# Kernel tuning notes

Hardware: AMD Instinct MI355X
Metric: run time of the kernel (lower is better)

Reference implementation:

```python
import jax, jax.numpy as jnp
import numpy as np

L = 3          # atom_decoder_depth
HEADS = 8      # spatial attention heads
T_HEADS = 8    # temporal attention heads
WQ = 32        # atoms_per_window_queries
HK = 128       # atoms_per_window_keys
EPS = 1e-5


def _ln(x, g=None, b=None):
    mu = jnp.mean(x, -1, keepdims=True)
    v = jnp.mean((x - mu) ** 2, -1, keepdims=True)
    xn = (x - mu) * jax.lax.rsqrt(v + EPS)
    if g is not None:
        xn = xn * g + b
    return xn


def _adaln(a, s, w_sc, b_sc, w_sk):
    # adaptive LN: sigmoid-scaled normed activations + conditioned skip
    sn = _ln(s)
    return jax.nn.sigmoid(sn @ w_sc + b_sc) * _ln(a) + sn @ w_sk


def setup_inputs() -> dict:
    key = jax.random.key(0)
    ks = iter(jax.random.split(key, 64))
    B0, T, N, M, D, TS = 1, 8, 1024, 4096, 256, 768
    HID = 2 * D

    def rn(shape, s=1.0):
        return jax.random.normal(next(ks), shape, jnp.float32) * s

    NW = (M + WQ - 1) // WQ
    a = rn((B0 * T, N, 2 * TS))
    q = rn((B0 * T, M, D))
    c = rn((B0 * T, M, D))
    atom_dec_bias = rn((B0, NW, WQ, HK, L * HEADS), 0.1)
    tok_idx = jnp.sort(jax.random.randint(next(ks), (B0, M), 0, N), axis=-1)
    atom_to_token = jax.nn.one_hot(tok_idx, N, dtype=jnp.float32)
    atom_pad_mask = jnp.ones((B0, M), bool)
    timestamps = jnp.sort(jax.random.uniform(next(ks), (B0, T)) * 10.0, axis=-1)
    p = 0.02
    return dict(
        a=a, q=q, c=c, atom_dec_bias=atom_dec_bias,
        atom_to_token=atom_to_token, atom_pad_mask=atom_pad_mask,
        timestamps=timestamps,
        W_a2q=rn((2 * TS, D), p),
        ada1_sw=rn((L, D, D), p), ada1_sb=rn((L, D), p), ada1_kw=rn((L, D, D), p),
        attn_wq=rn((L, D, D), p), attn_bq=rn((L, D), p),
        attn_wk=rn((L, D, D), p), attn_wv=rn((L, D, D), p),
        attn_wg=rn((L, D, D), p), attn_wo=rn((L, D, D), p),
        og_w=rn((L, D, D), p), og_b=rn((L, D), p),
        ada2_sw=rn((L, D, D), p), ada2_sb=rn((L, D), p), ada2_kw=rn((L, D, D), p),
        tr_w1=rn((L, D, HID), p), tr_w2=rn((L, D, HID), p), tr_w3=rn((L, HID, D), p),
        tr_gw=rn((L, D, D), p), tr_gb=rn((L, D), p),
        t_ln_g=jnp.ones((L, D)), t_ln_b=jnp.zeros((L, D)),
        t_wq=rn((L, D, D), p), t_wk=rn((L, D, D), p), t_wv=rn((L, D, D), p),
        t_wg=rn((L, D, D), p), t_wo=rn((L, D, D), p),
        t_decay=rn((L, T_HEADS)),
        pos_g=jnp.ones((D,)), pos_b=jnp.zeros((D,)), pos_w=rn((D, 3), p),
        T=8,
    )


def _forward(a, q, c, atom_dec_bias, atom_to_token, atom_pad_mask, timestamps,
             W_a2q, ada1_sw, ada1_sb, ada1_kw, attn_wq, attn_bq, attn_wk,
             attn_wv, attn_wg, attn_wo, og_w, og_b, ada2_sw, ada2_sb, ada2_kw,
             tr_w1, tr_w2, tr_w3, tr_gw, tr_gb, t_ln_g, t_ln_b, t_wq, t_wk,
             t_wv, t_wg, t_wo, t_decay, pos_g, pos_b, pos_w, T):
    BT, N, _ = a.shape
    B0 = BT // T
    M0, D = q.shape[1], q.shape[2]
    NW = (M0 + WQ - 1) // WQ
    M = NW * WQ
    h, dh = HEADS, D // HEADS
    th, tdh = T_HEADS, D // T_HEADS

    # token -> atom gather via one-hot matmul (atom_to_token shared across T)
    a2q = jnp.einsum('bmn,btnd->btmd', atom_to_token,
                     (a @ W_a2q).reshape(B0, T, N, D)).reshape(BT, M0, D)
    q = q + a2q

    pad = M - M0
    qf = jnp.pad(q, ((0, 0), (0, pad), (0, 0)))
    cf = jnp.pad(c, ((0, 0), (0, pad), (0, 0)))
    mask = jnp.pad(atom_pad_mask, ((0, 0), (0, pad)))  # (B0, M)

    side = (HK - WQ) // 2
    # index map: query window w attends keys [w*WQ - side, w*WQ - side + HK)
    widx = jnp.arange(NW)[:, None] * WQ + jnp.arange(HK)[None, :]

    def window_keys(x):  # (B, M, D) -> (B, NW, HK, D)
        xp = jnp.pad(x, ((0, 0), (side, side), (0, 0)))
        return xp[:, widx]

    kmask = jnp.pad(mask, ((0, 0), (side, side)))[:, widx]  # (B0, NW, HK)
    neg = jnp.where(kmask[:, None, :, None, None, :], 0.0, -1e9)

    bias = atom_dec_bias.reshape(B0, NW, WQ, HK, L, HEADS)
    inv_s = 1.0 / np.sqrt(dh).astype(np.float32)
    inv_t = 1.0 / np.sqrt(tdh).astype(np.float32)
    dt = jnp.abs(timestamps[:, :, None] - timestamps[:, None, :])  # (B0,T,T)

    for i in range(L):
        # ---- spatial windowed attention with pair bias ----
        b = _adaln(qf, cf, ada1_sw[i], ada1_sb[i], ada1_kw[i])
        qh = (b @ attn_wq[i] + attn_bq[i]).reshape(BT, NW, WQ, h, dh)
        kin = window_keys(b)                                   # (BT,NW,HK,D)
        kh = (kin @ attn_wk[i]).reshape(BT, NW, HK, h, dh)
        vh = (kin @ attn_wv[i]).reshape(BT, NW, HK, h, dh)
        logits = jnp.einsum('bnqhd,bnkhd->bnhqk', qh, kh) * inv_s
        logits = logits.reshape(B0, T, NW, h, WQ, HK)
        logits = logits + bias[:, :, :, :, i].transpose(0, 1, 4, 2, 3)[:, None] + neg
        p_attn = jax.nn.softmax(logits, axis=-1).reshape(BT, NW, h, WQ, HK)
        o = jnp.einsum('bnhqk,bnkhd->bnqhd', p_attn, vh)
        g = jax.nn.sigmoid(b @ attn_wg[i]).reshape(BT, NW, WQ, h, dh)
        o = (g * o).reshape(BT, M, D) @ attn_wo[i]
        qf = qf + jax.nn.sigmoid(cf @ og_w[i] + og_b[i]) * o
        # conditioned SwiGLU transition
        t = _adaln(qf, cf, ada2_sw[i], ada2_sb[i], ada2_kw[i])
        x = jax.nn.silu(t @ tr_w1[i]) * (t @ tr_w2[i])
        qf = qf + jax.nn.sigmoid(cf @ tr_gw[i] + tr_gb[i]) * (x @ tr_w3[i])
        # ---- temporal attention with per-head decay bias ----
        xt = qf.reshape(B0, T, M, D).transpose(0, 2, 1, 3)     # (B0,M,T,D)
        xn = _ln(xt, t_ln_g[i], t_ln_b[i])
        tq = (xn @ t_wq[i]).reshape(B0, M, T, th, tdh)
        tk = (xn @ t_wk[i]).reshape(B0, M, T, th, tdh)
        tv = (xn @ t_wv[i]).reshape(B0, M, T, th, tdh)
        tl = jnp.einsum('bmqhd,bmkhd->bmhqk', tq, tk) * inv_t
        decay = jax.nn.softplus(t_decay[i])                    # (th,)
        tl = tl - decay[None, None, :, None, None] * dt[:, None, None]
        tp = jax.nn.softmax(tl, axis=-1)
        to = jnp.einsum('bmhqk,bmkhd->bmqhd', tp, tv).reshape(B0, M, T, D)
        tg = jax.nn.sigmoid(xn @ t_wg[i])
        xt = xt + (tg * to) @ t_wo[i]
        qf = xt.transpose(0, 2, 1, 3).reshape(BT, M, D)

    q_out = qf[:, :M0]
    return _ln(q_out, pos_g, pos_b) @ pos_w  # (B*T, M0, 3)


def reference(a, q, c, atom_dec_bias, atom_to_token, atom_pad_mask, timestamps,
              W_a2q, ada1_sw, ada1_sb, ada1_kw, attn_wq, attn_bq, attn_wk,
              attn_wv, attn_wg, attn_wo, og_w, og_b, ada2_sw, ada2_sb, ada2_kw,
              tr_w1, tr_w2, tr_w3, tr_gw, tr_gb, t_ln_g, t_ln_b, t_wq, t_wk,
              t_wv, t_wg, t_wo, t_decay, pos_g, pos_b, pos_w, T):
    return _forward(a, q, c, atom_dec_bias, atom_to_token, atom_pad_mask,
                    timestamps, W_a2q, ada1_sw, ada1_sb, ada1_kw, attn_wq,
                    attn_bq, attn_wk, attn_wv, attn_wg, attn_wo, og_w, og_b,
                    ada2_sw, ada2_sb, ada2_kw, tr_w1, tr_w2, tr_w3, tr_gw,
                    tr_gb, t_ln_g, t_ln_b, t_wq, t_wk, t_wv, t_wg, t_wo,
                    t_decay, pos_g, pos_b, pos_w, T)
```

## Files before the change

### kernel.cpp

```cpp
#include <hip/hip_runtime.h>
#include <cstddef>
#include <cstdint>

#define DEVI __device__ __forceinline__

typedef __attribute__((ext_vector_type(8))) __bf16 bf16x8;
typedef __attribute__((ext_vector_type(8))) unsigned short us8;
typedef __attribute__((ext_vector_type(4))) unsigned short us4;
typedef __attribute__((ext_vector_type(4))) float f32x4;

constexpr int B0_ = 1, T_ = 8, N_ = 1024, M_ = 4096, D_ = 256;
constexpr int BT_ = 8, NW_ = 128, WQ_ = 32, HK_ = 128, SIDE_ = 48;
constexpr int R_ = BT_ * M_;
constexpr size_t Fq = 8388608;

DEVI unsigned short f2b(float f) {
  return __builtin_bit_cast(unsigned short, static_cast<__bf16>(f));
}
DEVI float b2f(unsigned short s) { return __uint_as_float(((unsigned)s) << 16); }
DEVI float sigm(float x) { return 1.0f / (1.0f + __expf(-x)); }
DEVI bf16x8 ld_bf8(const unsigned short* p) {
  return __builtin_bit_cast(bf16x8, *(const us8*)p);
}
DEVI bf16x8 pack_f8(float4 v0, float4 v1) {
  bf16x8 r;
  r[0] = (__bf16)v0.x; r[1] = (__bf16)v0.y; r[2] = (__bf16)v0.z; r[3] = (__bf16)v0.w;
  r[4] = (__bf16)v1.x; r[5] = (__bf16)v1.y; r[6] = (__bf16)v1.z; r[7] = (__bf16)v1.w;
  return r;
}
DEVI void mfma_bf16(f32x4& c, bf16x8 a, bf16x8 b) {
  c = __builtin_amdgcn_mfma_f32_16x16x32_bf16(a, b, c, 0, 0, 0);
}
DEVI void gload16(const void* g, void* l) {
  __builtin_amdgcn_global_load_lds((__attribute__((address_space(1))) void*)g,
                                   (__attribute__((address_space(3))) void*)l, 16, 0, 0);
}

struct ConvArgs {
  const float* src[64];
  int doff[64];
  int Kd[64];
  int Nd[64];
  int n;
};

__global__ __launch_bounds__(256) void conv_k(ConvArgs ca, unsigned short* __restrict__ wbf) {
  int e = blockIdx.x;
  int K = ca.Kd[e], N = ca.Nd[e];
  int nx = N >> 6, nk = K >> 6;
  int t = blockIdx.y;
  if (t >= nx * nk) return;
  int tx = t % nx, tk = t / nx;
  const float* s = ca.src[e];
  unsigned short* d = wbf + ca.doff[e];
  int n = tx * 64 + (threadIdx.x & 63);
  int k0 = tk * 64 + (threadIdx.x >> 6) * 16;
  for (int r = 0; r < 16; r++) {
    int k = k0 + r;
    d[(size_t)n * K + k] = f2b(s[(size_t)k * N + n]);
  }
}

__global__ __launch_bounds__(256) void cvt_k(const float* __restrict__ s,
                                             unsigned short* __restrict__ d, int n8) {
  int i = blockIdx.x * 256 + threadIdx.x;
  if (i >= n8) return;
  float4 v0 = *(const float4*)(s + (size_t)i * 8);
  float4 v1 = *(const float4*)(s + (size_t)i * 8 + 4);
  *(us8*)(d + (size_t)i * 8) = __builtin_bit_cast(us8, pack_f8(v0, v1));
}

__global__ __launch_bounds__(256) void bias_prep_k(
    const float* __restrict__ bq, const float* __restrict__ sb1,
    const float* __restrict__ sb2, const float* __restrict__ ogb,
    const float* __restrict__ trb, float* __restrict__ bias) {
  int t = threadIdx.x;
  for (int i = t; i < 1024 + 3 * 2560; i += 256) bias[i] = 0.f;
  __syncthreads();
  for (int i = 0; i < 3; i++) {
    float* B = bias + 1024 + i * 2560;
    B[t]        = bq[i * 256 + t];
    B[1024 + t] = sb1[i * 256 + t];
    B[1536 + t] = sb2[i * 256 + t];
    B[2048 + t] = ogb[i * 256 + t];
    B[2304 + t] = trb[i * 256 + t];
  }
}

__global__ __launch_bounds__(256) void biasb_k(const float* __restrict__ adb,
                                               unsigned short* __restrict__ biasb) {
  __shared__ float ld[3072];
  int rq = blockIdx.x;
  int t = threadIdx.x;
  const float* src = adb + (size_t)rq * 3072;
  for (int i = t; i < 3072; i += 256) ld[i] = src[i];
  __syncthreads();
  int k = t & 127;
  for (int lh = t >> 7; lh < 24; lh += 2)
    biasb[((size_t)lh * 4096 + rq) * 128 + k] = f2b(ld[k * 24 + lh]);
}

__global__ __launch_bounds__(256) void tokidx_k(const float* __restrict__ a2t,
                                                int* __restrict__ idx) {
  int m = blockIdx.x * 4 + (threadIdx.x >> 6);
  int lane = threadIdx.x & 63;
  int best = -1;
  for (int j = 0; j < 16; j++) {
    int col = lane * 16 + j;
    if (a2t[(size_t)m * 1024 + col] > 0.5f) best = col;
  }
#pragma unroll
  for (int off = 1; off < 64; off <<= 1) best = max(best, __shfl_xor(best, off));
  if (lane == 0) idx[m] = best;
}

__global__ __launch_bounds__(256) void qfinitln_k(const float* __restrict__ q,
                                                  const unsigned short* __restrict__ tokf,
                                                  const int* __restrict__ idx,
                                                  float* __restrict__ qf,
                                                  unsigned short* __restrict__ lnout) {
  int wid = threadIdx.x >> 6, lane = threadIdx.x & 63;
  size_t row = (size_t)blockIdx.x * 4 + wid;
  int m = (int)(row & 4095);
  int bt = (int)(row >> 12);
  float4 qv = *(const float4*)(q + row * 256 + lane * 4);
  us4 tv = *(const us4*)(tokf + ((size_t)bt * 1024 + idx[m]) * 256 + lane * 4);
  float x[4];
  x[0] = qv.x + b2f(tv[0]); x[1] = qv.y + b2f(tv[1]);
  x[2] = qv.z + b2f(tv[2]); x[3] = qv.w + b2f(tv[3]);
  *(float4*)(qf + row * 256 + lane * 4) = make_float4(x[0], x[1], x[2], x[3]);
  float s = x[0] + x[1] + x[2] + x[3];
  float sq = x[0] * x[0] + x[1] * x[1] + x[2] * x[2] + x[3] * x[3];
#pragma unroll
  for (int o = 1; o < 64; o <<= 1) {
    s += __shfl_xor(s, o);
    sq += __shfl_xor(sq, o);
  }
  float mu = s * 0.00390625f;
  float rs = rsqrtf(sq * 0.00390625f - mu * mu + 1e-5f);
  us4 r;
#pragma unroll
  for (int j = 0; j < 4; j++) r[j] = f2b((x[j] - mu) * rs);
  *(us4*)(lnout + row * 256 + lane * 4) = r;
}

__global__ __launch_bounds__(256) void ln_k(const float* __restrict__ src,
                                            unsigned short* __restrict__ dst) {
  size_t row = (size_t)blockIdx.x * 4 + (threadIdx.x >> 6);
  int lane = threadIdx.x & 63;
  float4 v = ((const float4*)(src + row * 256))[lane];
  float s = v.x + v.y + v.z + v.w;
#pragma unroll
  for (int o = 1; o < 64; o <<= 1) s += __shfl_xor(s, o);
  float mu = s * 0.00390625f;
  float dx = v.x - mu, dy = v.y - mu, dz = v.z - mu, dw = v.w - mu;
  float qv = dx * dx + dy * dy + dz * dz + dw * dw;
#pragma unroll
  for (int o = 1; o < 64; o <<= 1) qv += __shfl_xor(qv, o);
  float rs = rsqrtf(qv * 0.00390625f + 1e-5f);
  us4 r;
  r[0] = f2b(dx * rs); r[1] = f2b(dy * rs); r[2] = f2b(dz * rs); r[3] = f2b(dw * rs);
  *(us4*)(dst + row * 256 + lane * 4) = r;
}

template <int K, int EP, int PAIR>
__global__ __launch_bounds__(256) void gemm4_k(
    const unsigned short* __restrict__ A, const unsigned short* __restrict__ Wt,
    const float* __restrict__ bias, unsigned short* __restrict__ out,
    const unsigned short* __restrict__ lnq, int NOUT) {
  constexpr int NT = K / 64;
  __shared__ __align__(16) unsigned short S[2][16384];
  const int tid = threadIdx.x;
  const int lane = tid & 63, w = tid >> 6;
  const int lg = lane >> 4, lr = lane & 15;
  const int wr = w >> 1, wc = w & 1;
  const size_t m_base = (size_t)blockIdx.x * 128;
  const size_t n_base = (size_t)blockIdx.y * 64;
  const int srow = w * 8 + (lane >> 3);
  const int scol = ((lane & 7) ^ (lane >> 3)) * 8;
  const unsigned short* gA = A + (m_base + srow) * K + scol;
  const unsigned short* gB = Wt + (n_base + srow) * K + scol;
  const unsigned short* gB2 = Wt + (n_base + PAIR + srow) * K + scol;
  f32x4 acc[4][2] = {};
  f32x4 acc2[4][2] = {};
  const int swz = lr & 7;

  auto stage = [&](int buf, int t) {
    unsigned short* Sb = S[buf];
    const int kk = t * 64;
#pragma unroll
    for (int j = 0; j < 4; j++)
      gload16(gA + (size_t)(j * 32) * K + kk, Sb + w * 512 + j * 2048);
#pragma unroll
    for (int j = 0; j < 2; j++)
      gload16(gB + (size_t)(j * 32) * K + kk, Sb + 8192 + w * 512 + j * 2048);
#pragma unroll
    for (int j = 0; j < 2; j++)
      gload16(gB2 + (size_t)(j * 32) * K + kk, Sb + 12288 + w * 512 + j * 2048);
  };
  auto compute = [&](int buf) {
    const unsigned short* Sb = S[buf];
#pragma unroll
    for (int ks = 0; ks < 2; ks++) {
      const int co = ((ks * 4 + lg) ^ swz) << 3;
      bf16x8 af[4], b1[2], b2[2];
#pragma unroll
      for (int i = 0; i < 4; i++)
        af[i] = ld_bf8(Sb + (wr * 64 + i * 16 + lr) * 64 + co);
#pragma unroll
      for (int i = 0; i < 2; i++) {
        b1[i] = ld_bf8(Sb + 8192 + (wc * 32 + i * 16 + lr) * 64 + co);
        b2[i] = ld_bf8(Sb + 12288 + (wc * 32 + i * 16 + lr) * 64 + co);
      }
#pragma unroll
      for (int mi = 0; mi < 4; mi++)
#pragma unroll
        for (int ni = 0; ni < 2; ni++) {
          mfma_bf16(acc[mi][ni], af[mi], b1[ni]);
          mfma_bf16(acc2[mi][ni], af[mi], b2[ni]);
        }
    }
  };

  stage(0, 0);
  __syncthreads();
  int cur = 0;
  for (int t = 0; t < NT - 1; t++) {
    stage(cur ^ 1, t + 1);
    compute(cur);
    __syncthreads();
    cur ^= 1;
  }
  compute(cur);
  __syncthreads();

  unsigned short* St = S[0];
  if constexpr (EP == 1) {
#pragma unroll
    for (int half = 0; half < 2; half++) {
      int cbase = (int)n_base + half * PAIR;
#pragma unroll
      for (int mi = 0; mi < 4; mi++)
#pragma unroll
        for (int ni = 0; ni < 2; ni++)
#pragma unroll
          for (int r = 0; r < 4; r++) {
            int rowl = wr * 64 + mi * 16 + lg * 4 + r;
            int cl = wc * 32 + ni * 16 + lr;
            float v = (half ? acc2[mi][ni][r] : acc[mi][ni][r]) + bias[cbase + cl];
            St[rowl * 64 + (((cl >> 3) ^ (rowl & 7)) << 3) + (cl & 7)] = f2b(v);
          }
      __syncthreads();
#pragma unroll
      for (int p = 0; p < 4; p++) {
        int rowl = p * 32 + (tid >> 3);
        int chunk = tid & 7;
        us8 v = *(const us8*)(St + rowl * 64 + ((chunk ^ (rowl & 7)) << 3));
        *(us8*)(out + (m_base + rowl) * NOUT + cbase + chunk * 8) = v;
      }
      __syncthreads();
    }
  } else {
#pragma unroll
    for (int mi = 0; mi < 4; mi++)
#pragma unroll
      for (int ni = 0; ni < 2; ni++)
#pragma unroll
        for (int r = 0; r < 4; r++) {
          int rowl = wr * 64 + mi * 16 + lg * 4 + r;
          int cl = wc * 32 + ni * 16 + lr;
          size_t grow = m_base + rowl;
          int gcol = (int)n_base + cl;
          float v = acc[mi][ni][r] + bias[gcol];
          float v2 = acc2[mi][ni][r] + bias[gcol + PAIR];
          unsigned short res;
          if constexpr (EP == 4) {
            res = f2b(sigm(v) * b2f(lnq[grow * 256 + gcol]) + v2);
          } else {
            res = f2b(v * sigm(v) * v2);
          }
          St[rowl * 64 + (((cl >> 3) ^ (rowl & 7)) << 3) + (cl & 7)] = res;
        }
    __syncthreads();
#pragma unroll
    for (int p = 0; p < 4; p++) {
      int rowl = p * 32 + (tid >> 3);
      int chunk = tid & 7;
      us8 v = *(const us8*)(St + rowl * 64 + ((chunk ^ (rowl & 7)) << 3));
      *(us8*)(out + (m_base + rowl) * NOUT + n_base + chunk * 8) = v;
    }
  }
}

template <int K, bool GATED>
__global__ __launch_bounds__(512) void gemmln_k(
    const unsigned short* __restrict__ A, const unsigned short* __restrict__ Wt,
    float* __restrict__ qf, const unsigned short* __restrict__ gate, int goff,
    unsigned short* __restrict__ lnout, const float* __restrict__ lng,
    const float* __restrict__ lnb) {
  constexpr int NT = K / 64;
  __shared__ __align__(16) unsigned short S[2][20480];
  const int tid = threadIdx.x;
  const int lane = tid & 63, w = tid >> 6;
  const int lg = lane >> 4, lr = lane & 15;
  const size_t m_base = (size_t)blockIdx.x * 64;
  const int srow = lane >> 3;
  const int scol = ((lane & 7) ^ srow) * 8;
  const unsigned short* gA = A + (m_base + w * 8 + srow) * K + scol;
  const unsigned short* gB = Wt + (w * 32 + srow) * K + scol;
  f32x4 acc[4][2] = {};
  const int swz = lr & 7;

  auto stage = [&](int buf, int t) {
    unsigned short* Sb = S[buf];
    const int kk = t * 64;
    gload16(gA + kk, Sb + w * 512);
#pragma unroll
    for (int j = 0; j < 4; j++)
      gload16(gB + (size_t)(j * 8) * K + kk, Sb + 4096 + w * 2048 + j * 512);
  };
  auto compute = [&](int buf) {
    const unsigned short* Sb = S[buf];
#pragma unroll
    for (int ks = 0; ks < 2; ks++) {
      const int co = ((ks * 4 + lg) ^ swz) << 3;
      bf16x8 af[4], bf1[2];
#pragma unroll
      for (int i = 0; i < 4; i++) af[i] = ld_bf8(Sb + (i * 16 + lr) * 64 + co);
#pragma unroll
      for (int i = 0; i < 2; i++)
        bf1[i] = ld_bf8(Sb + 4096 + (w * 32 + i * 16 + lr) * 64 + co);
#pragma unroll
      for (int mi = 0; mi < 4; mi++)
#pragma unroll
        for (int ni = 0; ni < 2; ni++) mfma_bf16(acc[mi][ni], af[mi], bf1[ni]);
    }
  };

  stage(0, 0);
  __syncthreads();
  int cur = 0;
  for (int t = 0; t < NT - 1; t++) {
    stage(cur ^ 1, t + 1);
    compute(cur);
    __syncthreads();
    cur ^= 1;
  }
  compute(cur);
  __syncthreads();

  unsigned short* St = S[0];
#pragma unroll
  for (int mi = 0; mi < 4; mi++)
#pragma unroll
    for (int ni = 0; ni < 2; ni++)
#pragma unroll
      for (int r = 0; r < 4; r++) {
        int rowl = mi * 16 + lg * 4 + r;
        int col = w * 32 + ni * 16 + lr;
        size_t grow = m_base + rowl;
        float v = acc[mi][ni][r];
        if constexpr (GATED) v *= sigm(b2f(gate[grow * 512 + goff + col]));
        float nq = qf[grow * 256 + col] + v;
        qf[grow * 256 + col] = nq;
        St[rowl * 256 + (((col >> 3) ^ (rowl & 7)) << 3) + (col & 7)] = f2b(nq);
      }
  __syncthreads();
  float gv[4], bv[4];
  if (lng) {
#pragma unroll
    for (int j = 0; j < 4; j++) {
      gv[j] = lng[lane * 4 + j];
      bv[j] = lnb[lane * 4 + j];
    }
  }
  const int rchunk = lane >> 1;
  const int rsub = (lane & 1) << 2;
  for (int rr = 0; rr < 8; rr++) {
    int rowl = w * 8 + rr;
    us4 vv = *(const us4*)(St + rowl * 256 + ((rchunk ^ (rowl & 7)) << 3) + rsub);
    float x[4];
#pragma unroll
    for (int j = 0; j < 4; j++) x[j] = b2f(vv[j]);
    float s = x[0] + x[1] + x[2] + x[3];
    float sq = x[0] * x[0] + x[1] * x[1] + x[2] * x[2] + x[3] * x[3];
#pragma unroll
    for (int o = 1; o < 64; o <<= 1) {
      s += __shfl_xor(s, o);
      sq += __shfl_xor(sq, o);
    }
    float mu = s * 0.00390625f;
    float rs = rsqrtf(sq * 0.00390625f - mu * mu + 1e-5f);
    us4 r;
#pragma unroll
    for (int j = 0; j < 4; j++) {
      float y = (x[j] - mu) * rs;
      if (lng) y = y * gv[j] + bv[j];
      r[j] = f2b(y);
    }
    *(us4*)(lnout + (m_base + rowl) * 256 + lane * 4) = r;
  }
}

__global__ __launch_bounds__(256) void attn_k(const unsigned short* __restrict__ big1,
                                              const unsigned short* __restrict__ biasb,
                                              unsigned short* __restrict__ o, int layer) {
  __shared__ __align__(16) unsigned short pl_s[4][32 * 128];
  __shared__ __align__(16) unsigned short vt_s[4][32 * 128];
  const int w = blockIdx.x, bt = blockIdx.y, hg = blockIdx.z;
  const int tid = threadIdx.x, wid = tid >> 6, lane = tid & 63;
  const int lg = lane >> 4, lr = lane & 15;
  const int h = hg * 4 + wid;
  unsigned short* pl = pl_s[wid];
  unsigned short* vt = vt_s[wid];
  const size_t base = (size_t)bt * M_;
  const float inv_s = 0.17677669529663687f;

  {
    const int chunk = lane & 3;
    const int krow = lane >> 2;
#pragma unroll
    for (int it = 0; it < 8; it++) {
      int key = it * 16 + krow;
      int ak = w * 32 - SIDE_ + key;
      int akc = ak < 0 ? 0 : (ak > M_ - 1 ? M_ - 1 : ak);
      us8 v = *(const us8*)(big1 + (base + akc) * 1024 + 512 + h * 32 + chunk * 8);
#pragma unroll
      for (int e = 0; e < 8; e++) {
        int d = chunk * 8 + e;
        vt[d * 128 + (key ^ ((d & 7) << 3))] = v[e];
      }
    }
  }
  bf16x8 aq[2];
#pragma unroll
  for (int mi = 0; mi < 2; mi++)
    aq[mi] = ld_bf8(big1 + (base + w * 32 + mi * 16 + lr) * 1024 + h * 32 + lg * 8);
  f32x4 lac[2][8] = {};
#pragma unroll
  for (int ni = 0; ni < 8; ni++) {
    int kidx = ni * 16 + lr;
    int ak = w * 32 - SIDE_ + kidx;
    int akc = ak < 0 ? 0 : (ak > M_ - 1 ? M_ - 1 : ak);
    bf16x8 bk = ld_bf8(big1 + (base + akc) * 1024 + 256 + h * 32 + lg * 8);
    mfma_bf16(lac[0][ni], aq[0], bk);
    mfma_bf16(lac[1][ni], aq[1], bk);
  }
  const unsigned short* brow0 =
      biasb + (((size_t)(layer * 8 + h)) * 4096 + w * 32) * 128;
#pragma unroll
  for (int mi = 0; mi < 2; mi++)
#pragma unroll
    for (int r = 0; r < 4; r++) {
      int qrow = mi * 16 + lg * 4 + r;
      const unsigned short* brow = brow0 + (size_t)qrow * 128;
      float lv[8];
      float mx = -3e38f;
#pragma unroll
      for (int ni = 0; ni < 8; ni++) {
        int kidx = ni * 16 + lr;
        int ak = w * 32 - SIDE_ + kidx;
        float x = lac[mi][ni][r] * inv_s + b2f(brow[kidx]) +
                  ((unsigned)ak < (unsigned)M_ ? 0.f : -1e9f);
        lv[ni] = x;
        mx = fmaxf(mx, x);
      }
#pragma unroll
      for (int off = 1; off < 16; off <<= 1) mx = fmaxf(mx, __shfl_xor(mx, off));
      float sum = 0.f;
#pragma unroll
      for (int ni = 0; ni < 8; ni++) {
        float e = __expf(lv[ni] - mx);
        lv[ni] = e;
        sum += e;
      }
#pragma unroll
      for (int off = 1; off < 16; off <<= 1) sum += __shfl_xor(sum, off);
      float inv = 1.f / sum;
      int sw = (qrow & 7) << 3;
#pragma unroll
      for (int ni = 0; ni < 8; ni++)
        pl[qrow * 128 + ((ni * 16 + lr) ^ sw)] = f2b(lv[ni] * inv);
    }
  f32x4 oc[2][2] = {};
#pragma unroll
  for (int ks = 0; ks < 4; ks++) {
    int kbase = ks * 32 + lg * 8;
    int kswz = kbase ^ ((lr & 7) << 3);
    bf16x8 ap0 = ld_bf8(pl + lr * 128 + kswz);
    bf16x8 ap1 = ld_bf8(pl + (16 + lr) * 128 + kswz);
    bf16x8 bv0 = ld_bf8(vt + lr * 128 + kswz);
    bf16x8 bv1 = ld_bf8(vt + (16 + lr) * 128 + kswz);
    mfma_bf16(oc[0][0], ap0, bv0);
    mfma_bf16(oc[0][1], ap0, bv1);
    mfma_bf16(oc[1][0], ap1, bv0);
    mfma_bf16(oc[1][1], ap1, bv1);
  }
#pragma unroll
  for (int mi = 0; mi < 2; mi++)
#pragma unroll
    for (int nd = 0; nd < 2; nd++)
#pragma unroll
      for (int r = 0; r < 4; r++) {
        int qrow = mi * 16 + lg * 4 + r;
        int d = nd * 16 + lr;
        size_t rowi = base + w * 32 + qrow;
        float gv = sigm(b2f(big1[rowi * 1024 + 768 + h * 32 + d]));
        o[rowi * 256 + h * 32 + d] = f2b(oc[mi][nd][r] * gv);
      }
}

__global__ __launch_bounds__(256) void tattn_k(const unsigned short* __restrict__ big1,
                                               const float* __restrict__ ts,
                                               const float* __restrict__ tdec,
                                               unsigned short* __restrict__ o, int layer) {
  __shared__ __align__(16) unsigned short lds[4][8 * 768];
  int wid = threadIdx.x >> 6, lane = threadIdx.x & 63;
  int m = blockIdx.x * 4 + wid;
  unsigned short* Lp = lds[wid];
  for (int it = 0; it < 12; it++) {
    int u = it * 64 + lane;
    int t = u / 96, pos = (u % 96) * 8;
    *(uint4*)(Lp + t * 768 + pos) =
        *(const uint4*)(big1 + ((size_t)(t * M_ + m)) * 1024 + pos);
  }
  __syncthreads();
  int th = lane >> 3, qt = lane & 7;
  float decay = log1pf(__expf(tdec[layer * 8 + th]));
  float tsq = ts[qt];
  const float inv_t = 0.17677669529663687f;
  float tqv[32];
#pragma unroll
  for (int d = 0; d < 32; d++) tqv[d] = b2f(Lp[qt * 768 + th * 32 + d]);
  float lv[8];
  float mx = -3e38f;
#pragma unroll
  for (int kt = 0; kt < 8; kt++) {
    float dot = 0.f;
#pragma unroll
    for (int d = 0; d < 32; d++) dot += tqv[d] * b2f(Lp[kt * 768 + 256 + th * 32 + d]);
    float x = dot * inv_t - decay * fabsf(tsq - ts[kt]);
    lv[kt] = x;
    mx = fmaxf(mx, x);
  }
  float s = 0.f;
#pragma unroll
  for (int kt = 0; kt < 8; kt++) {
    float e = __expf(lv[kt] - mx);
    lv[kt] = e;
    s += e;
  }
  float inv = 1.f / s;
  float tov[32];
#pragma unroll
  for (int d = 0; d < 32; d++) tov[d] = 0.f;
#pragma unroll
  for (int kt = 0; kt < 8; kt++) {
    float p = lv[kt] * inv;
#pragma unroll
    for (int d = 0; d < 32; d++) tov[d] += p * b2f(Lp[kt * 768 + 512 + th * 32 + d]);
  }
  size_t orow = (size_t)qt * M_ + m;
#pragma unroll
  for (int d = 0; d < 32; d++) {
    float tg = sigm(b2f(big1[orow * 1024 + 768 + th * 32 + d]));
    o[orow * 256 + th * 32 + d] = f2b(tov[d] * tg);
  }
}

__global__ __launch_bounds__(256) void final_k(const float* __restrict__ qf,
                                               const float* __restrict__ pg,
                                               const float* __restrict__ pb,
                                               const float* __restrict__ pw,
                                               float* __restrict__ out) {
  size_t row = (size_t)blockIdx.x * 4 + (threadIdx.x >> 6);
  int lane = threadIdx.x & 63;
  float4 v = ((const float4*)(qf + row * 256))[lane];
  float s = v.x + v.y + v.z + v.w;
#pragma unroll
  for (int o = 1; o < 64; o <<= 1) s += __shfl_xor(s, o);
  float mu = s * 0.00390625f;
  float dx = v.x - mu, dy = v.y - mu, dz = v.z - mu, dw = v.w - mu;
  float qv = dx * dx + dy * dy + dz * dz + dw * dw;
#pragma unroll
  for (int o = 1; o < 64; o <<= 1) qv += __shfl_xor(qv, o);
  float rs = rsqrtf(qv * 0.00390625f + 1e-5f);
  int d = lane * 4;
  float xn[4];
  xn[0] = dx * rs * pg[d] + pb[d];
  xn[1] = dy * rs * pg[d + 1] + pb[d + 1];
  xn[2] = dz * rs * pg[d + 2] + pb[d + 2];
  xn[3] = dw * rs * pg[d + 3] + pb[d + 3];
  float p0 = 0.f, p1 = 0.f, p2 = 0.f;
#pragma unroll
  for (int dd = 0; dd < 4; dd++) {
    const float* wr = pw + (size_t)(d + dd) * 3;
    p0 += xn[dd] * wr[0];
    p1 += xn[dd] * wr[1];
    p2 += xn[dd] * wr[2];
  }
#pragma unroll
  for (int o = 1; o < 64; o <<= 1) {
    p0 += __shfl_xor(p0, o);
    p1 += __shfl_xor(p1, o);
    p2 += __shfl_xor(p2, o);
  }
  if (lane == 0) {
    out[row * 3 + 0] = p0;
    out[row * 3 + 1] = p1;
    out[row * 3 + 2] = p2;
  }
}

extern "C" void kernel_launch(void* const* d_in, const int* in_sizes, int n_in,
                              void* d_out, int out_size, void* d_ws, size_t ws_size,
                              hipStream_t stream) {
  const float* a       = (const float*)d_in[0];
  const float* q_in    = (const float*)d_in[1];
  const float* c_in    = (const float*)d_in[2];
  const float* adb     = (const float*)d_in[3];
  const float* a2t     = (const float*)d_in[4];
  const float* ts      = (const float*)d_in[6];
  const float* W_a2q   = (const float*)d_in[7];
  const float* ada1_sw = (const float*)d_in[8];
  const float* ada1_sb = (const float*)d_in[9];
  const float* ada1_kw = (const float*)d_in[10];
  const float* attn_wq = (const float*)d_in[11];
  const float* attn_bq = (const float*)d_in[12];
  const float* attn_wk = (const float*)d_in[13];
  const float* attn_wv = (const float*)d_in[14];
  const float* attn_wg = (const float*)d_in[15];
  const float* attn_wo = (const float*)d_in[16];
  const float* og_w    = (const float*)d_in[17];
  const float* og_b    = (const float*)d_in[18];
  const float* ada2_sw = (const float*)d_in[19];
  const float* ada2_sb = (const float*)d_in[20];
  const float* ada2_kw = (const float*)d_in[21];
  const float* tr_w1   = (const float*)d_in[22];
  const float* tr_w2   = (const float*)d_in[23];
  const float* tr_w3   = (const float*)d_in[24];
  const float* tr_gw   = (const float*)d_in[25];
  const float* tr_gb   = (const float*)d_in[26];
  const float* t_ln_g  = (const float*)d_in[27];
  const float* t_ln_b  = (const float*)d_in[28];
  const float* t_wq    = (const float*)d_in[29];
  const float* t_wk    = (const float*)d_in[30];
  const float* t_wv    = (const float*)d_in[31];
  const float* t_wg    = (const float*)d_in[32];
  const float* t_wo    = (const float*)d_in[33];
  const float* t_dec   = (const float*)d_in[34];
  const float* pos_g   = (const float*)d_in[35];
  const float* pos_b   = (const float*)d_in[36];
  const float* pos_w   = (const float*)d_in[37];

  char* base = (char*)d_ws;
  size_t off = 0;
  auto alloc = [&](size_t bytes) {
    void* p = base + off;
    off += (bytes + 255) & ~(size_t)255;
    return p;
  };
  float* qf            = (float*)alloc(Fq * 4);
  unsigned short* lncb = (unsigned short*)alloc(Fq * 2);
  unsigned short* lnqb = (unsigned short*)alloc(Fq * 2);
  unsigned short* obuf = (unsigned short*)alloc(Fq * 2);
  unsigned short* big1 = (unsigned short*)alloc(Fq * 8);
  unsigned short* bbuf = (unsigned short*)alloc(Fq * 2);
  unsigned short* cbf  = (unsigned short*)alloc(Fq * 2);
  unsigned short* biasb= (unsigned short*)alloc((size_t)24 * 4096 * 128 * 2);
  unsigned short* wbf  = (unsigned short*)alloc((size_t)4718592 * 2);
  float* biasr         = (float*)alloc(8704 * 4);
  int* tokidx          = (int*)alloc(4096 * 4);

  unsigned short* xbuf  = big1;
  unsigned short* ggate = big1 + (size_t)R_ * 512;
  unsigned short* abf   = big1;
  unsigned short* tokf  = big1 + 2 * Fq;

  ConvArgs ca;
  int ne = 0;
  auto add = [&](const float* s, size_t doff, int K, int N) {
    ca.src[ne] = s; ca.doff[ne] = (int)doff; ca.Kd[ne] = K; ca.Nd[ne] = N; ne++;
  };
  constexpr size_t LW = 1441792;
  for (int i = 0; i < 3; i++) {
    size_t LB = (size_t)i * LW;
    add(ada1_sw + i * 65536, LB + 0, 256, 256);
    add(ada1_kw + i * 65536, LB + 65536, 256, 256);
    add(attn_wq + i * 65536, LB + 131072, 256, 256);
    add(attn_wk + i * 65536, LB + 196608, 256, 256);
    add(attn_wv + i * 65536, LB + 262144, 256, 256);
    add(attn_wg + i * 65536, LB + 327680, 256, 256);
    add(attn_wo + i * 65536, LB + 393216, 256, 256);
    add(og_w + i * 65536, LB + 458752, 256, 256);
    add(tr_gw + i * 65536, LB + 524288, 256, 256);
    add(ada2_sw + i * 65536, LB + 589824, 256, 256);
    add(ada2_kw + i * 65536, LB + 655360, 256, 256);
    add(tr_w1 + i * 131072, LB + 720896, 256, 512);
    add(tr_w2 + i * 131072, LB + 851968, 256, 512);
    add(tr_w3 + i * 131072, LB + 983040, 512, 256);
    add(t_wq + i * 65536, LB + 1114112, 256, 256);
    add(t_wk + i * 65536, LB + 1179648, 256, 256);
    add(t_wv + i * 65536, LB + 1245184, 256, 256);
    add(t_wg + i * 65536, LB + 1310720, 256, 256);
    add(t_wo + i * 65536, LB + 1376256, 256, 256);
  }
  add(W_a2q, 3 * LW, 1536, 256);
  ca.n = ne;

  conv_k<<<dim3(ne, 96), 256, 0, stream>>>(ca, wbf);
  bias_prep_k<<<1, 256, 0, stream>>>(attn_bq, ada1_sb, ada2_sb, og_b, tr_gb, biasr);
  tokidx_k<<<1024, 256, 0, stream>>>(a2t, tokidx);
  biasb_k<<<4096, 256, 0, stream>>>(adb, biasb);
  cvt_k<<<6144, 256, 0, stream>>>(a, abf, 1572864);
  cvt_k<<<4096, 256, 0, stream>>>(c_in, cbf, 1048576);
  gemm4_k<1536, 1, 128><<<dim3(64, 2), 256, 0, stream>>>(
      abf, wbf + 3 * LW, biasr, tokf, nullptr, 256);
  qfinitln_k<<<8192, 256, 0, stream>>>(q_in, tokf, tokidx, qf, lnqb);
  ln_k<<<8192, 256, 0, stream>>>(c_in, lncb);

  for (int i = 0; i < 3; i++) {
    size_t LB = (size_t)i * LW;
    const float* b_attn = biasr + 1024 + (size_t)i * 2560;
    const float* b_ada1 = b_attn + 1024;
    const float* b_ada2 = b_attn + 1536;
    const float* b_ogtr = b_attn + 2048;

    gemm4_k<256, 4, 256><<<dim3(256, 4), 256, 0, stream>>>(
        lncb, wbf + LB, b_ada1, bbuf, lnqb, 256);
    gemm4_k<256, 1, 512><<<dim3(256, 8), 256, 0, stream>>>(
        bbuf, wbf + LB + 131072, b_attn, big1, nullptr, 1024);
    attn_k<<<dim3(128, 8, 2), 256, 0, stream>>>(big1, biasb, obuf, i);
    gemm4_k<256, 1, 256><<<dim3(256, 4), 256, 0, stream>>>(
        cbf, wbf + LB + 458752, b_ogtr, ggate, nullptr, 512);
    gemmln_k<256, true><<<512, 512, 0, stream>>>(
        obuf, wbf + LB + 393216, qf, ggate, 0, lnqb, nullptr, nullptr);
    gemm4_k<256, 4, 256><<<dim3(256, 4), 256, 0, stream>>>(
        lncb, wbf + LB + 589824, b_ada2, bbuf, lnqb, 256);
    gemm4_k<256, 5, 512><<<dim3(256, 8), 256, 0, stream>>>(
        bbuf, wbf + LB + 720896, biasr, xbuf, nullptr, 512);
    gemmln_k<512, true><<<512, 512, 0, stream>>>(
        xbuf, wbf + LB + 983040, qf, ggate, 256, lnqb,
        t_ln_g + (size_t)i * 256, t_ln_b + (size_t)i * 256);
    gemm4_k<256, 1, 512><<<dim3(256, 8), 256, 0, stream>>>(
        lnqb, wbf + LB + 1114112, biasr, big1, nullptr, 1024);
    tattn_k<<<1024, 256, 0, stream>>>(big1, ts, t_dec, obuf, i);
    gemmln_k<256, false><<<512, 512, 0, stream>>>(
        obuf, wbf + LB + 1376256, qf, nullptr, 0, lnqb, nullptr, nullptr);
  }
  final_k<<<8192, 256, 0, stream>>>(qf, pos_g, pos_b, pos_w, (float*)d_out);
}
```

Before: 1.153 ms.

## Emit transposed V from projection GEMM and permute bias layout for attention

Result: no change. 1.144 ms (-0.8%).

```diff
diff --git a/kernel.cpp b/kernel.cpp
--- a/kernel.cpp
+++ b/kernel.cpp
@@ -96,8 +96,9 @@
   for (int i = t; i < 3072; i += 256) ld[i] = src[i];
   __syncthreads();
   int k = t & 127;
+  int pk = (k & 15) * 8 + (k >> 4);
   for (int lh = t >> 7; lh < 24; lh += 2)
-    biasb[((size_t)lh * 4096 + rq) * 128 + k] = f2b(ld[k * 24 + lh]);
+    biasb[((size_t)lh * 4096 + rq) * 128 + pk] = f2b(ld[k * 24 + lh]);
 }
 
 __global__ __launch_bounds__(256) void tokidx_k(const float* __restrict__ a2t,
@@ -167,7 +168,8 @@
 __global__ __launch_bounds__(256) void gemm4_k(
     const unsigned short* __restrict__ A, const unsigned short* __restrict__ Wt,
     const float* __restrict__ bias, unsigned short* __restrict__ out,
-    const unsigned short* __restrict__ lnq, int NOUT) {
+    const unsigned short* __restrict__ lnq, unsigned short* __restrict__ vtb,
+    int NOUT) {
   constexpr int NT = K / 64;
   __shared__ __align__(16) unsigned short S[2][16384];
   const int tid = threadIdx.x;
@@ -235,30 +237,59 @@
   __syncthreads();
 
   unsigned short* St = S[0];
+  auto emit_half = [&](int cbase, bool second) {
+#pragma unroll
+    for (int mi = 0; mi < 4; mi++)
+#pragma unroll
+      for (int ni = 0; ni < 2; ni++)
+#pragma unroll
+        for (int r = 0; r < 4; r++) {
+          int rowl = wr * 64 + mi * 16 + lg * 4 + r;
+          int cl = wc * 32 + ni * 16 + lr;
+          float v = (second ? acc2[mi][ni][r] : acc[mi][ni][r]) + bias[cbase + cl];
+          St[rowl * 64 + (((cl >> 3) ^ (rowl & 7)) << 3) + (cl & 7)] = f2b(v);
+        }
+    __syncthreads();
+#pragma unroll
+    for (int p = 0; p < 4; p++) {
+      int rowl = p * 32 + (tid >> 3);
+      int chunk = tid & 7;
+      us8 v = *(const us8*)(St + rowl * 64 + ((chunk ^ (rowl & 7)) << 3));
+      *(us8*)(out + (m_base + rowl) * NOUT + cbase + chunk * 8) = v;
+    }
+    __syncthreads();
+  };
+
   if constexpr (EP == 1) {
-#pragma unroll
-    for (int half = 0; half < 2; half++) {
-      int cbase = (int)n_base + half * PAIR;
+    emit_half((int)n_base, false);
+    emit_half((int)n_base + PAIR, true);
+  } else if constexpr (EP == 6) {
+    emit_half((int)n_base, false);
+    if ((int)n_base < 256) {
+      const int bt = (int)(m_base >> 12);
+      const int m0 = (int)(m_base & 4095);
 #pragma unroll
       for (int mi = 0; mi < 4; mi++)
 #pragma unroll
-        for (int ni = 0; ni < 2; ni++)
-#pragma unroll
-          for (int r = 0; r < 4; r++) {
-            int rowl = wr * 64 + mi * 16 + lg * 4 + r;
-            int cl = wc * 32 + ni * 16 + lr;
-            float v = (half ? acc2[mi][ni][r] : acc[mi][ni][r]) + bias[cbase + cl];
-            St[rowl * 64 + (((cl >> 3) ^ (rowl & 7)) << 3) + (cl & 7)] = f2b(v);
-          }
+        for (int ni = 0; ni < 2; ni++) {
+          int cl = wc * 32 + ni * 16 + lr;
+          int rowb = wr * 64 + mi * 16 + lg * 4;
+          us4 val;
+#pragma unroll
+          for (int r = 0; r < 4; r++)
+            val[r] = f2b(acc2[mi][ni][r] + bias[(int)n_base + cl + 512]);
+          *(us4*)(St + cl * 128 + (((rowb >> 3) ^ (cl & 7)) << 3) + (rowb & 7)) = val;
+        }
       __syncthreads();
 #pragma unroll
       for (int p = 0; p < 4; p++) {
-        int rowl = p * 32 + (tid >> 3);
-        int chunk = tid & 7;
-        us8 v = *(const us8*)(St + rowl * 64 + ((chunk ^ (rowl & 7)) << 3));
-        *(us8*)(out + (m_base + rowl) * NOUT + cbase + chunk * 8) = v;
+        int cl = tid >> 2;
+        int rc = (tid & 3) + p * 4;
+        us8 v = *(const us8*)(St + cl * 128 + ((rc ^ (cl & 7)) << 3));
+        *(us8*)(vtb + ((size_t)bt * 256 + n_base + cl) * 4096 + m0 + rc * 8) = v;
       }
-      __syncthreads();
+    } else {
+      emit_half((int)n_base + 512, true);
     }
   } else {
 #pragma unroll
@@ -403,11 +434,14 @@
 }
 
 __global__ __launch_bounds__(256) void attn_k(const unsigned short* __restrict__ big1,
+                                              const unsigned short* __restrict__ vtbuf,
                                               const unsigned short* __restrict__ biasb,
                                               unsigned short* __restrict__ o, int layer) {
   __shared__ __align__(16) unsigned short pl_s[4][32 * 128];
   __shared__ __align__(16) unsigned short vt_s[4][32 * 128];
-  const int w = blockIdx.x, bt = blockIdx.y, hg = blockIdx.z;
+  const int bid = blockIdx.x;
+  const int nid = (bid & 7) * 256 + (bid >> 3);
+  const int w = nid & 127, bt = (nid >> 7) & 7, hg = nid >> 10;
   const int tid = threadIdx.x, wid = tid >> 6, lane = tid & 63;
   const int lg = lane >> 4, lr = lane & 15;
   const int h = hg * 4 + wid;
@@ -417,19 +451,17 @@
   const float inv_s = 0.17677669529663687f;
 
   {
-    const int chunk = lane & 3;
-    const int krow = lane >> 2;
-#pragma unroll
-    for (int it = 0; it < 8; it++) {
-      int key = it * 16 + krow;
-      int ak = w * 32 - SIDE_ + key;
-      int akc = ak < 0 ? 0 : (ak > M_ - 1 ? M_ - 1 : ak);
-      us8 v = *(const us8*)(big1 + (base + akc) * 1024 + 512 + h * 32 + chunk * 8);
-#pragma unroll
-      for (int e = 0; e < 8; e++) {
-        int d = chunk * 8 + e;
-        vt[d * 128 + (key ^ ((d & 7) << 3))] = v[e];
-      }
+    const int d = lane >> 1, half = lane & 1;
+    const unsigned short* src = vtbuf + ((size_t)bt * 256 + h * 32 + d) * 4096;
+    const int k0 = w * 32 - SIDE_ + half * 64;
+    unsigned short* dst = vt + d * 128;
+#pragma unroll
+    for (int c = 0; c < 8; c++) {
+      int ak = k0 + c * 8;
+      ak = ak < 0 ? 0 : (ak > M_ - 8 ? M_ - 8 : ak);
+      us8 v = *(const us8*)(src + ak);
+      const int chunk = half * 8 + c;
+      *(us8*)(dst + ((chunk ^ (d & 7)) << 3)) = v;
     }
   }
   bf16x8 aq[2];
@@ -446,21 +478,20 @@
     mfma_bf16(lac[0][ni], aq[0], bk);
     mfma_bf16(lac[1][ni], aq[1], bk);
   }
-  const unsigned short* brow0 =
-      biasb + (((size_t)(layer * 8 + h)) * 4096 + w * 32) * 128;
+  const unsigned short* bb0 =
+      biasb + (((size_t)(layer * 8 + h)) * 4096 + w * 32) * 128 + lr * 8;
 #pragma unroll
   for (int mi = 0; mi < 2; mi++)
 #pragma unroll
     for (int r = 0; r < 4; r++) {
       int qrow = mi * 16 + lg * 4 + r;
-      const unsigned short* brow = brow0 + (size_t)qrow * 128;
+      us8 bb = *(const us8*)(bb0 + (size_t)qrow * 128);
       float lv[8];
       float mx = -3e38f;
 #pragma unroll
       for (int ni = 0; ni < 8; ni++) {
-        int kidx = ni * 16 + lr;
-        int ak = w * 32 - SIDE_ + kidx;
-        float x = lac[mi][ni][r] * inv_s + b2f(brow[kidx]) +
+        int ak = w * 32 - SIDE_ + ni * 16 + lr;
+        float x = lac[mi][ni][r] * inv_s + b2f(bb[ni]) +
                   ((unsigned)ak < (unsigned)M_ ? 0.f : -1e9f);
         lv[ni] = x;
         mx = fmaxf(mx, x);
@@ -667,6 +698,7 @@
   unsigned short* big1 = (unsigned short*)alloc(Fq * 8);
   unsigned short* bbuf = (unsigned short*)alloc(Fq * 2);
   unsigned short* cbf  = (unsigned short*)alloc(Fq * 2);
+  unsigned short* vtbuf= (unsigned short*)alloc(Fq * 2);
   unsigned short* biasb= (unsigned short*)alloc((size_t)24 * 4096 * 128 * 2);
   unsigned short* wbf  = (unsigned short*)alloc((size_t)4718592 * 2);
   float* biasr         = (float*)alloc(8704 * 4);
@@ -715,7 +747,7 @@
   cvt_k<<<6144, 256, 0, stream>>>(a, abf, 1572864);
   cvt_k<<<4096, 256, 0, stream>>>(c_in, cbf, 1048576);
   gemm4_k<1536, 1, 128><<<dim3(64, 2), 256, 0, stream>>>(
-      abf, wbf + 3 * LW, biasr, tokf, nullptr, 256);
+      abf, wbf + 3 * LW, biasr, tokf, nullptr, nullptr, 256);
   qfinitln_k<<<8192, 256, 0, stream>>>(q_in, tokf, tokidx, qf, lnqb);
   ln_k<<<8192, 256, 0, stream>>>(c_in, lncb);
 
@@ -727,23 +759,23 @@
     const float* b_ogtr = b_attn + 2048;
 
     gemm4_k<256, 4, 256><<<dim3(256, 4), 256, 0, stream>>>(
-        lncb, wbf + LB, b_ada1, bbuf, lnqb, 256);
-    gemm4_k<256, 1, 512><<<dim3(256, 8), 256, 0, stream>>>(
-        bbuf, wbf + LB + 131072, b_attn, big1, nullptr, 1024);
-    attn_k<<<dim3(128, 8, 2), 256, 0, stream>>>(big1, biasb, obuf, i);
+        lncb, wbf + LB, b_ada1, bbuf, lnqb, nullptr, 256);
+    gemm4_k<256, 6, 512><<<dim3(256, 8), 256, 0, stream>>>(
+        bbuf, wbf + LB + 131072, b_attn, big1, nullptr, vtbuf, 1024);
+    attn_k<<<2048, 256, 0, stream>>>(big1, vtbuf, biasb, obuf, i);
     gemm4_k<256, 1, 256><<<dim3(256, 4), 256, 0, stream>>>(
-        cbf, wbf + LB + 458752, b_ogtr, ggate, nullptr, 512);
+        cbf, wbf + LB + 458752, b_ogtr, ggate, nullptr, nullptr, 512);
     gemmln_k<256, true><<<512, 512, 0, stream>>>(
         obuf, wbf + LB + 393216, qf, ggate, 0, lnqb, nullptr, nullptr);
     gemm4_k<256, 4, 256><<<dim3(256, 4), 256, 0, stream>>>(
-        lncb, wbf + LB + 589824, b_ada2, bbuf, lnqb, 256);
+        lncb, wbf + LB + 589824, b_ada2, bbuf, lnqb, nullptr, 256);
     gemm4_k<256, 5, 512><<<dim3(256, 8), 256, 0, stream>>>(
-        bbuf, wbf + LB + 720896, biasr, xbuf, nullptr, 512);
+        bbuf, wbf + LB + 720896, biasr, xbuf, nullptr, nullptr, 512);
     gemmln_k<512, true><<<512, 512, 0, stream>>>(
         xbuf, wbf + LB + 983040, qf, ggate, 256, lnqb,
         t_ln_g + (size_t)i * 256, t_ln_b + (size_t)i * 256);
     gemm4_k<256, 1, 512><<<dim3(256, 8), 256, 0, stream>>>(
-        lnqb, wbf + LB + 1114112, biasr, big1, nullptr, 1024);
+        lnqb, wbf + LB + 1114112, biasr, big1, nullptr, nullptr, 1024);
     tattn_k<<<1024, 256, 0, stream>>>(big1, ts, t_dec, obuf, i);
     gemmln_k<256, false><<<512, 512, 0, stream>>>(
         obuf, wbf + LB + 1376256, qf, nullptr, 0, lnqb, nullptr, nullptr);
```
